# Performance work log

Hardware: AMD Instinct MI355X
Metric: run time of the kernel (lower is better)

## Reference

```python
import jax, jax.numpy as jnp
import numpy as np

N = 20000      # points
K = 16         # neighbor pairs per query per branch
M = N * K      # total pairs
C = 384        # embed_dim
H = 6          # num_heads
HD = C // H    # head_dim = 64
H1 = H // 2    # cartesian-branch heads
L = 24         # quant_grid_length (window 6.0 / quant 0.25)
Q = 0.25       # quant_size
LS = 24        # quant_grid_length_sphere (120 / 5)
QS = 5.0       # quant_size_sphere
A = 0.05 * 0.25  # exponential_split 'a'
SCALE = HD ** -0.5


def setup_inputs() -> dict:
    key = jax.random.key(0)
    ks = jax.random.split(key, 12)
    s = 0.02
    inp = {}
    inp["query_feats"] = jax.random.normal(ks[0], (N, C), jnp.float32)
    inp["xyz"] = jax.random.uniform(ks[1], (N, 3), jnp.float32, -3.0, 3.0)
    inp["index_0"] = jnp.repeat(jnp.arange(N, dtype=jnp.int32), K)
    inp["index_1"] = jax.random.randint(ks[2], (M,), 0, N, dtype=jnp.int32)
    inp["index_0_sphere"] = jnp.repeat(jnp.arange(N, dtype=jnp.int32), K)
    inp["index_1_sphere"] = jax.random.randint(ks[3], (M,), 0, N, dtype=jnp.int32)
    inp["W_qkv"] = jax.random.normal(ks[4], (C, 3 * C), jnp.float32) * s
    inp["b_qkv"] = jnp.zeros((3 * C,), jnp.float32)
    inp["W_proj"] = jax.random.normal(ks[5], (C, C), jnp.float32) * s
    inp["b_proj"] = jnp.zeros((C,), jnp.float32)
    inp["tq"] = jax.random.normal(ks[6], (2 * L - 1, 3, H1, HD), jnp.float32) * s
    inp["tk"] = jax.random.normal(ks[7], (2 * L - 1, 3, H1, HD), jnp.float32) * s
    inp["tv"] = jax.random.normal(ks[8], (2 * L - 1, 3, H1, HD), jnp.float32) * s
    inp["tq_s"] = jax.random.normal(ks[9], (2 * LS, 3, H - H1, HD), jnp.float32) * s
    inp["tk_s"] = jax.random.normal(ks[10], (2 * LS, 3, H - H1, HD), jnp.float32) * s
    inp["tv_s"] = jax.random.normal(ks[11], (2 * LS, 3, H - H1, HD), jnp.float32) * s
    return inp


def _cart2sphere(xyz):
    x, y, z = xyz[:, 0], xyz[:, 1], xyz[:, 2]
    theta = (jnp.arctan2(y, x) + np.pi) * (180.0 / np.pi)
    beta = jnp.arctan2(jnp.sqrt(x * x + y * y), z) * (180.0 / np.pi)
    r = jnp.sqrt(x * x + y * y + z * z)
    return jnp.stack([theta, beta, r], -1)


def _rel_idx_cart(xyz, i0, i1):
    rel = xyz[i0] - xyz[i1]  # [M,3]
    idx = jnp.floor(rel / Q).astype(jnp.int32) + (L - 1)
    return jnp.clip(idx, 0, 2 * L - 2)


def _rel_idx_sphere(sph, i0, i1):
    rel = sph[i0] - sph[i1]  # [M,3] (theta, beta, r)
    idx01 = jnp.clip(jnp.floor(rel[:, :2] / QS).astype(jnp.int32) + LS, 0, 2 * LS - 1)
    # exponential_split on radial dim
    r = rel[:, 2]
    ra = jnp.abs(r)
    flag = (r >= 0).astype(jnp.float32)
    idx = 2.0 * jnp.floor(jnp.log((ra + 2.0 * A) / A) / np.log(2.0)) - 2.0
    idx = idx + ((3.0 * jnp.exp2(jnp.floor(idx / 2.0)) - 2.0) * A <= ra).astype(jnp.float32)
    idx = idx * (2.0 * flag - 1.0) + (flag - 1.0)
    idx2 = jnp.clip(idx.astype(jnp.int32) + 24, 0, 2 * LS - 1)
    return jnp.concatenate([idx01, idx2[:, None]], 1)


def _branch(q, k, v, i0, i1, rel_idx, Tq, Tk, Tv):
    # q,k,v: [N,h,d]; i0/i1: [M]; rel_idx: [M,3]; tables: [R,3,h,d]
    qg = q[i0]  # [M,h,d]
    kg = k[i1]
    attn = jnp.einsum('mhd,mhd->mh', qg, kg)
    for dim in range(3):
        attn = attn + jnp.einsum('mhd,mhd->mh', qg, Tq[rel_idx[:, dim], dim])
        attn = attn + jnp.einsum('mhd,mhd->mh', kg, Tk[rel_idx[:, dim], dim])
    # segment softmax over queries (i0)
    seg_max = jax.ops.segment_max(attn, i0, num_segments=N)
    ex = jnp.exp(attn - seg_max[i0])
    p = ex / jax.ops.segment_sum(ex, i0, num_segments=N)[i0]  # [M,h]
    vg = v[i1] + Tv[rel_idx[:, 0], 0] + Tv[rel_idx[:, 1], 1] + Tv[rel_idx[:, 2], 2]
    return jax.ops.segment_sum(p[:, :, None] * vg, i0, num_segments=N)  # [N,h,d]


def reference(query_feats, xyz, index_0, index_1, index_0_sphere, index_1_sphere,
              W_qkv, b_qkv, W_proj, b_proj, tq, tk, tv, tq_s, tk_s, tv_s):
    i0 = index_0.astype(jnp.int32)
    i1 = index_1.astype(jnp.int32)
    i0s = index_0_sphere.astype(jnp.int32)
    i1s = index_1_sphere.astype(jnp.int32)
    qkv = (query_feats @ W_qkv + b_qkv).reshape(N, 3, H, HD)
    q = qkv[:, 0] * SCALE
    k = qkv[:, 1]
    v = qkv[:, 2]
    sph = _cart2sphere(xyz)
    ri = _rel_idx_cart(xyz, i0, i1)
    out1 = _branch(q[:, :H1], k[:, :H1], v[:, :H1], i0, i1, ri, tq, tk, tv)
    ri_s = _rel_idx_sphere(sph, i0s, i1s)
    out2 = _branch(q[:, H1:], k[:, H1:], v[:, H1:], i0s, i1s, ri_s, tq_s, tk_s, tv_s)
    x = jnp.concatenate([out1, out2], 1).reshape(N, C)
    return x @ W_proj + b_proj
```

## Files before the change

kernel.cpp:

```cpp
#include <hip/hip_runtime.h>
#include <hip/hip_bf16.h>

namespace {

constexpr int NP   = 20000;
constexpr int CD   = 384;
constexpr int QKVD = 1152;
constexpr int TC   = 47 * 3 * 3 * 64;
constexpr int TS   = 48 * 3 * 3 * 64;

constexpr int PB0 = NP * CD / 4 / 256;
constexpr int PB1 = PB0 + (QKVD / 32) * (CD / 32);
constexpr int PB2 = PB1 + (CD / 32) * (CD / 32);
constexpr int PB3 = PB2 + 27 * 7;

constexpr int ANB = 240;
constexpr int ANY = (NP + ANB - 1) / ANB;

typedef __attribute__((ext_vector_type(8))) short short8;
typedef __attribute__((ext_vector_type(4))) float f32x4;
typedef __attribute__((ext_vector_type(2))) float f32x2;

__device__ inline float f32_atan2(float y, float x) {
  return (float)atan2((double)y, (double)x);
}
__device__ inline float f32_log(float x) {
  return (float)log((double)x);
}

__device__ inline float bfl(unsigned u) {
  union { unsigned u; float f; } c; c.u = u << 16; return c.f;
}
__device__ inline float bfh(unsigned u) {
  union { unsigned u; float f; } c; c.u = u & 0xffff0000u; return c.f;
}
__device__ inline f32x2 up2(unsigned u) {
  f32x2 r;
  r.x = bfl(u);
  r.y = bfh(u);
  return r;
}
__device__ inline unsigned short f2bf(float x) {
  __hip_bfloat16 hb = __float2bfloat16(x);
  unsigned short u; __builtin_memcpy(&u, &hb, 2);
  return u;
}

#if __has_builtin(__builtin_amdgcn_fdot2_f32_bf16)
#define HAVE_BF16_DOT 1
typedef __attribute__((ext_vector_type(2))) __bf16 bf16x2_t;
__device__ inline float dot2bf(unsigned a, unsigned b, float c) {
  bf16x2_t av, bv;
  __builtin_memcpy(&av, &a, 4);
  __builtin_memcpy(&bv, &b, 4);
  return __builtin_amdgcn_fdot2_f32_bf16(av, bv, c, false);
}
#endif

__device__ inline void async16(const void* g, void* l) {
  __builtin_amdgcn_global_load_lds(
      (const __attribute__((address_space(1))) unsigned int*)g,
      (__attribute__((address_space(3))) unsigned int*)l,
      16, 0, 0);
}

__device__ inline uint4 tld(const char* t, int row, int bo) {
  return *(const uint4*)(t + row * 128 + (bo ^ ((row & 7) << 4)));
}
__device__ inline void tst(char* t, int row, int bo, uint4 v) {
  *(uint4*)(t + row * 128 + (bo ^ ((row & 7) << 4))) = v;
}

__global__ __launch_bounds__(256) void prep_all_k(const float* __restrict__ qf,
                                                  unsigned short* __restrict__ qf_b,
                                                  const float* __restrict__ Wqkv,
                                                  unsigned short* __restrict__ wqkvT,
                                                  const float* __restrict__ Wproj,
                                                  unsigned short* __restrict__ wprojT,
                                                  const float* __restrict__ tq,
                                                  const float* __restrict__ tk,
                                                  const float* __restrict__ tv,
                                                  const float* __restrict__ tqs,
                                                  const float* __restrict__ tks,
                                                  const float* __restrict__ tvs,
                                                  unsigned short* __restrict__ tq_b,
                                                  unsigned short* __restrict__ tk_b,
                                                  unsigned short* __restrict__ tv_b,
                                                  unsigned short* __restrict__ tqs_b,
                                                  unsigned short* __restrict__ tks_b,
                                                  unsigned short* __restrict__ tvs_b,
                                                  const float* __restrict__ xyz,
                                                  float* __restrict__ sph) {
  const int bid = blockIdx.x;
  const int tid = threadIdx.x;
  __shared__ float t[32][33];

  if (bid < PB0) {
    int i = (bid * 256 + tid) * 4;
    float4 v = *(const float4*)(qf + i);
    ushort4 o;
    o.x = f2bf(v.x); o.y = f2bf(v.y); o.z = f2bf(v.z); o.w = f2bf(v.w);
    *(ushort4*)(qf_b + i) = o;
  } else if (bid < PB2) {
    const float* in;
    unsigned short* out;
    int R, Cc, bx, by;
    if (bid < PB1) {
      in = Wqkv; out = wqkvT; R = CD; Cc = QKVD;
      int tt = bid - PB0; bx = tt % (QKVD / 32); by = tt / (QKVD / 32);
    } else {
      in = Wproj; out = wprojT; R = CD; Cc = CD;
      int tt = bid - PB1; bx = tt % (CD / 32); by = tt / (CD / 32);
    }
    const int c0 = bx * 32, r0 = by * 32;
    const int tx = tid & 31, ty = tid >> 5;
    #pragma unroll
    for (int i = 0; i < 32; i += 8)
      t[ty + i][tx] = in[(size_t)(r0 + ty + i) * Cc + (c0 + tx)];
    __syncthreads();
    #pragma unroll
    for (int i = 0; i < 32; i += 8)
      out[(size_t)(c0 + ty + i) * R + (r0 + tx)] = f2bf(t[tx][ty + i]);
  } else {
    const int tt = bid - PB2;
    const int bx = tt % 27, y = tt / 27;
    const int th = bx * 256 + tid;
    if (y < 6) {
      const float* in = (y == 0) ? tq : (y == 1) ? tk : (y == 2) ? tv
                      : (y == 3) ? tqs : (y == 4) ? tks : tvs;
      unsigned short* out = (y == 0) ? tq_b : (y == 1) ? tk_b : (y == 2) ? tv_b
                          : (y == 3) ? tqs_b : (y == 4) ? tks_b : tvs_b;
      const int n = (y < 3) ? TC : TS;
      int i = th * 4;
      if (i < n) {
        float4 v = *(const float4*)(in + i);
        ushort4 o;
        o.x = f2bf(v.x); o.y = f2bf(v.y); o.z = f2bf(v.z); o.w = f2bf(v.w);
        *(ushort4*)(out + i) = o;
      }
    } else {
#pragma clang fp contract(off)
      #pragma unroll
      for (int r = 0; r < 4; ++r) {
        int i = th * 4 + r;
        if (i < NP) {
          const float PIF = 3.14159265358979323846f;
          const float R2D = 57.29577951308232f;
          float x = xyz[i * 3 + 0], yy = xyz[i * 3 + 1], z = xyz[i * 3 + 2];
          float sxy = x * x + yy * yy;
          sph[i * 3 + 0] = (f32_atan2(yy, x) + PIF) * R2D;
          sph[i * 3 + 1] = f32_atan2(sqrtf(sxy), z) * R2D;
          sph[i * 3 + 2] = sqrtf(sxy + z * z);
        }
      }
    }
  }
}

__global__ __launch_bounds__(256) void bin_k(const float* __restrict__ xyz,
                                             const float* __restrict__ sph,
                                             const int* __restrict__ nb_c,
                                             const int* __restrict__ nb_s,
                                             int4* __restrict__ ebuf) {
#pragma clang fp contract(off)
  const int t = blockIdx.x * 256 + threadIdx.x;
  if (t >= 2 * NP * 16) return;
  const int b   = t / (NP * 16);
  const int rem = t - b * NP * 16;
  const int n   = rem >> 4;
  const int e   = rem & 15;
  int4 o;
  if (b == 0) {
    const int i1 = nb_c[n * 16 + e];
    const float rel[3] = {xyz[n * 3 + 0] - xyz[i1 * 3 + 0],
                          xyz[n * 3 + 1] - xyz[i1 * 3 + 1],
                          xyz[n * 3 + 2] - xyz[i1 * 3 + 2]};
    int r[3];
    #pragma unroll
    for (int dim = 0; dim < 3; ++dim) {
      int idx = (int)floorf(rel[dim] * 4.0f) + 23;
      idx = min(max(idx, 0), 46);
      r[dim] = idx * 3 + dim;
    }
    o.x = r[0]; o.y = r[1]; o.z = r[2]; o.w = i1;
  } else {
    const int i1 = nb_s[n * 16 + e];
    const float d0 = sph[n * 3 + 0] - sph[i1 * 3 + 0];
    const float d1 = sph[n * 3 + 1] - sph[i1 * 3 + 1];
    const float dr = sph[n * 3 + 2] - sph[i1 * 3 + 2];
    int i0a = (int)floorf(d0 / 5.0f) + 24;
    int i1a = (int)floorf(d1 / 5.0f) + 24;
    const float ra = fabsf(dr);
    const float flag = (dr >= 0.0f) ? 1.0f : 0.0f;
    const float tt = (ra + 0.025f) / 0.0125f;
    const float wv = f32_log(tt) / 0.69314718055994531f;
    float fidx = 2.0f * floorf(wv) - 2.0f;
    fidx += ((3.0f * exp2f(floorf(fidx * 0.5f)) - 2.0f) * 0.0125f <= ra) ? 1.0f : 0.0f;
    fidx = fidx * (2.0f * flag - 1.0f) + (flag - 1.0f);
    int i2a = (int)fidx + 24;
    o.x = min(max(i0a, 0), 47) * 3 + 0;
    o.y = min(max(i1a, 0), 47) * 3 + 1;
    o.z = min(max(i2a, 0), 47) * 3 + 2;
    o.w = i1;
  }
  ebuf[t] = o;
}

template <int MODE>
__global__ __launch_bounds__(256) void gemm_async_k(const short* __restrict__ A,
                                                    const short* __restrict__ BT,
                                                    const float* __restrict__ bias,
                                                    void* __restrict__ Cout,
                                                    int M, int Nn, int K) {
  __shared__ short As[3][128][32];
  __shared__ short Bs[3][128][32];
  const int tid  = threadIdx.x;

  const int NT  = Nn >> 7;
  const int nwg = gridDim.x;
  const int q = nwg >> 3, r = nwg & 7;
  const int xcd = blockIdx.x & 7, j = blockIdx.x >> 3;
  const int wg = (xcd < r ? xcd * (q + 1) : r * (q + 1) + (xcd - r) * q) + j;
  const int m0 = (wg / NT) * 128, n0 = (wg % NT) * 128;

  const int wave = tid >> 6, lane = tid & 63;
  const int wm   = (wave & 1) * 64, wn = (wave >> 1) * 64;
  const int quad = lane >> 4, l16 = lane & 15;
  const int srow = lane >> 2;
  const int scol = (lane & 3) * 8;

  f32x4 acc[4][4] = {};

  auto stage = [&](int buf, int k0) {
    #pragma unroll
    for (int c = 0; c < 2; ++c) {
      const int base = (wave + c * 4) * 16;
      async16(A + (size_t)(m0 + base + srow) * K + k0 + scol, &As[buf][base][0]);
      async16(BT + (size_t)(n0 + base + srow) * K + k0 + scol, &Bs[buf][base][0]);
    }
  };

  const int nt = K >> 5;
  stage(0, 0);
  stage(1, 32);
  for (int t = 0; t < nt; ++t) {
    const int cur = t % 3;
    if (t + 1 < nt) {
      asm volatile("s_waitcnt vmcnt(4)" ::: "memory");
    } else {
      asm volatile("s_waitcnt vmcnt(0)" ::: "memory");
    }
    __builtin_amdgcn_s_barrier();
    short8 af[4], bg[4];
    #pragma unroll
    for (int i = 0; i < 4; ++i) af[i] = *(const short8*)&As[cur][wm + i * 16 + l16][quad * 8];
    #pragma unroll
    for (int j2 = 0; j2 < 4; ++j2) bg[j2] = *(const short8*)&Bs[cur][wn + j2 * 16 + l16][quad * 8];
    #pragma unroll
    for (int i = 0; i < 4; ++i)
      #pragma unroll
      for (int j2 = 0; j2 < 4; ++j2)
        acc[i][j2] = __builtin_amdgcn_mfma_f32_16x16x32_bf16(af[i], bg[j2], acc[i][j2], 0, 0, 0);
    __builtin_amdgcn_s_barrier();
    if (t + 2 < nt) stage((t + 2) % 3, (t + 2) * 32);
  }

  #pragma unroll
  for (int i = 0; i < 4; ++i) {
    #pragma unroll
    for (int r2 = 0; r2 < 4; ++r2) {
      const int gm = m0 + wm + i * 16 + quad * 4 + r2;
      if (gm >= M) continue;
      #pragma unroll
      for (int j2 = 0; j2 < 4; ++j2) {
        const int gn = n0 + wn + j2 * 16 + l16;
        if (gn >= Nn) continue;
        float v = acc[i][j2][r2] + bias[gn];
        if (MODE == 0) {
          if (gn < 384) v *= 0.125f;
          ((unsigned short*)Cout)[(size_t)gm * Nn + gn] = f2bf(v);
        } else {
          ((float*)Cout)[(size_t)gm * Nn + gn] = v;
        }
      }
    }
  }
}

__device__ inline f32x2 dot8_pk(uint4 q, uint4 k, uint4 a0, uint4 a1, uint4 a2,
                                uint4 t0, uint4 t1, uint4 t2, f32x2 acc) {
  const unsigned* qp = &q.x;  const unsigned* kp = &k.x;
  const unsigned* a0p = &a0.x; const unsigned* a1p = &a1.x; const unsigned* a2p = &a2.x;
  const unsigned* t0p = &t0.x; const unsigned* t1p = &t1.x; const unsigned* t2p = &t2.x;
  #pragma unroll
  for (int w2 = 0; w2 < 4; ++w2) {
    f32x2 qf = up2(qp[w2]), kf = up2(kp[w2]);
    f32x2 tqs = up2(a0p[w2]) + up2(a1p[w2]) + up2(a2p[w2]);
    f32x2 tks = up2(t0p[w2]) + up2(t1p[w2]) + up2(t2p[w2]);
    acc += qf * (kf + tqs) + kf * tks;
  }
  return acc;
}

__device__ inline void acc4(f32x2* vc, uint4 vv, uint4 t0, uint4 t1, uint4 t2,
                            float pr) {
  f32x2 prv = {pr, pr};
  vc[0] += prv * (up2(vv.x) + up2(t0.x) + up2(t1.x) + up2(t2.x));
  vc[1] += prv * (up2(vv.y) + up2(t0.y) + up2(t1.y) + up2(t2.y));
  vc[2] += prv * (up2(vv.z) + up2(t0.z) + up2(t1.z) + up2(t2.z));
  vc[3] += prv * (up2(vv.w) + up2(t0.w) + up2(t1.w) + up2(t2.w));
}

__global__ __launch_bounds__(1024, 4) void attn_lds_k(const unsigned short* __restrict__ qkv,
                                                      const int4* __restrict__ ebuf,
                                                      const unsigned short* __restrict__ tq_c,
                                                      const unsigned short* __restrict__ tk_c,
                                                      const unsigned short* __restrict__ tv_c,
                                                      const unsigned short* __restrict__ tq_s,
                                                      const unsigned short* __restrict__ tk_s,
                                                      const unsigned short* __restrict__ tv_s,
                                                      unsigned short* __restrict__ xout) {
  __shared__ char s_tq[144 * 128];
  __shared__ char s_tk[144 * 128];
  __shared__ char s_tv[144 * 128];

  const int bh  = blockIdx.x;
  const int b   = bh / 3;
  const int hh  = bh % 3;
  const int wid = threadIdx.x >> 6, lane = threadIdx.x & 63;

  const unsigned short* gtq = b ? tq_s : tq_c;
  const unsigned short* gtk = b ? tk_s : tk_c;
  const unsigned short* gtv = b ? tv_s : tv_c;
  const int nrows = b ? 144 : 141;

  for (int i = threadIdx.x; i < nrows * 8; i += 1024) {
    const int row = i >> 3, c8 = i & 7;
    const int go = row * 192 + hh * 64 + c8 * 8;
    tst(s_tq, row, c8 * 16, *(const uint4*)(gtq + go));
    tst(s_tk, row, c8 * 16, *(const uint4*)(gtk + go));
    tst(s_tv, row, c8 * 16, *(const uint4*)(gtv + go));
  }
  __syncthreads();

  const int eg = lane >> 2, g = lane & 3;
  const int e8 = lane >> 3, c = lane & 7;
  const int node_end = min(blockIdx.y * ANB + ANB, NP);

  for (int node = blockIdx.y * ANB + wid; node < node_end; node += 16) {
    const int4* eb = ebuf + ((size_t)b * NP + node) * 16;

    const int4 E  = eb[eg];
    const int4 EA = eb[e8];
    const int4 EB = eb[e8 + 8];

    const unsigned short* qp = qkv + (size_t)node * QKVD + b * 192 + hh * 64 + g * 16;
    const uint4 qv0 = *(const uint4*)(qp);
    const uint4 qv1 = *(const uint4*)(qp + 8);
    const unsigned short* kp = qkv + (size_t)E.w * QKVD + 384 + b * 192 + hh * 64 + g * 16;
    const uint4 kv0 = *(const uint4*)(kp);
    const uint4 kv1 = *(const uint4*)(kp + 8);
    const int hc = hh * 64 + c * 8;
    const uint4 vA = *(const uint4*)(qkv + (size_t)EA.w * QKVD + 768 + b * 192 + hc);
    const uint4 vB = *(const uint4*)(qkv + (size_t)EB.w * QKVD + 768 + b * 192 + hc);

    const int bo = g * 32;
    const uint4 a00 = tld(s_tq, E.x, bo), a01 = tld(s_tq, E.x, bo + 16);
    const uint4 a10 = tld(s_tq, E.y, bo), a11 = tld(s_tq, E.y, bo + 16);
    const uint4 a20 = tld(s_tq, E.z, bo), a21 = tld(s_tq, E.z, bo + 16);
    const uint4 b00 = tld(s_tk, E.x, bo), b01 = tld(s_tk, E.x, bo + 16);
    const uint4 b10 = tld(s_tk, E.y, bo), b11 = tld(s_tk, E.y, bo + 16);
    const uint4 b20 = tld(s_tk, E.z, bo), b21 = tld(s_tk, E.z, bo + 16);

    float acc;
#ifdef HAVE_BF16_DOT
    float aqk = 0.0f, aq0 = 0.0f, aq1 = 0.0f, aq2 = 0.0f;
    float ak0 = 0.0f, ak1 = 0.0f, ak2 = 0.0f;
#define DOT7(qd, kd, a0d, a1d, a2d, b0d, b1d, b2d)                         \
    aqk = dot2bf(qd, kd, aqk);  aq0 = dot2bf(qd, a0d, aq0);                \
    aq1 = dot2bf(qd, a1d, aq1); aq2 = dot2bf(qd, a2d, aq2);                \
    ak0 = dot2bf(kd, b0d, ak0); ak1 = dot2bf(kd, b1d, ak1);                \
    ak2 = dot2bf(kd, b2d, ak2);
    DOT7(qv0.x, kv0.x, a00.x, a10.x, a20.x, b00.x, b10.x, b20.x)
    DOT7(qv0.y, kv0.y, a00.y, a10.y, a20.y, b00.y, b10.y, b20.y)
    DOT7(qv0.z, kv0.z, a00.z, a10.z, a20.z, b00.z, b10.z, b20.z)
    DOT7(qv0.w, kv0.w, a00.w, a10.w, a20.w, b00.w, b10.w, b20.w)
    DOT7(qv1.x, kv1.x, a01.x, a11.x, a21.x, b01.x, b11.x, b21.x)
    DOT7(qv1.y, kv1.y, a01.y, a11.y, a21.y, b01.y, b11.y, b21.y)
    DOT7(qv1.z, kv1.z, a01.z, a11.z, a21.z, b01.z, b11.z, b21.z)
    DOT7(qv1.w, kv1.w, a01.w, a11.w, a21.w, b01.w, b11.w, b21.w)
#undef DOT7
    acc = ((aqk + aq0) + (aq1 + aq2)) + ((ak0 + ak1) + ak2);
#else
    f32x2 acc2 = {0.0f, 0.0f};
    acc2 = dot8_pk(qv0, kv0, a00, a10, a20, b00, b10, b20, acc2);
    acc2 = dot8_pk(qv1, kv1, a01, a11, a21, b01, b11, b21, acc2);
    acc = acc2.x + acc2.y;
#endif
    acc += __shfl_xor(acc, 1);
    acc += __shfl_xor(acc, 2);

    float m = acc;
    #pragma unroll
    for (int off = 4; off <= 32; off <<= 1) m = fmaxf(m, __shfl_xor(m, off));
    float ex = __expf(acc - m);
    float s = ex;
    #pragma unroll
    for (int off = 4; off <= 32; off <<= 1) s += __shfl_xor(s, off);
    const float p = ex / s;

    const float pA = __shfl(p, e8 << 2);
    const float pB = __shfl(p, (e8 + 8) << 2);
    const int vbo = c * 16;
    const uint4 tA0 = tld(s_tv, EA.x, vbo);
    const uint4 tA1 = tld(s_tv, EA.y, vbo);
    const uint4 tA2 = tld(s_tv, EA.z, vbo);
    const uint4 tB0 = tld(s_tv, EB.x, vbo);
    const uint4 tB1 = tld(s_tv, EB.y, vbo);
    const uint4 tB2 = tld(s_tv, EB.z, vbo);

    f32x2 vc[4] = {{0.f, 0.f}, {0.f, 0.f}, {0.f, 0.f}, {0.f, 0.f}};
    acc4(vc, vA, tA0, tA1, tA2, pA);
    acc4(vc, vB, tB0, tB1, tB2, pB);

    #pragma unroll
    for (int q4 = 0; q4 < 4; ++q4) {
      #pragma unroll
      for (int off = 8; off <= 32; off <<= 1) {
        vc[q4].x += __shfl_xor(vc[q4].x, off);
        vc[q4].y += __shfl_xor(vc[q4].y, off);
      }
    }
    if (e8 == 0) {
      uint4 o;
      o.x = ((unsigned)f2bf(vc[0].y) << 16) | (unsigned)f2bf(vc[0].x);
      o.y = ((unsigned)f2bf(vc[1].y) << 16) | (unsigned)f2bf(vc[1].x);
      o.z = ((unsigned)f2bf(vc[2].y) << 16) | (unsigned)f2bf(vc[2].x);
      o.w = ((unsigned)f2bf(vc[3].y) << 16) | (unsigned)f2bf(vc[3].x);
      *(uint4*)(xout + (size_t)node * CD + (b * 3 + hh) * 64 + c * 8) = o;
    }
  }
}

}

extern "C" void kernel_launch(void* const* d_in, const int* in_sizes, int n_in,
                              void* d_out, int out_size, void* d_ws, size_t ws_size,
                              hipStream_t stream) {
  const float* qf    = (const float*)d_in[0];
  const float* xyz   = (const float*)d_in[1];
  const int*   i1c   = (const int*)d_in[3];
  const int*   i1s   = (const int*)d_in[5];
  const float* Wqkv  = (const float*)d_in[6];
  const float* bqkv  = (const float*)d_in[7];
  const float* Wproj = (const float*)d_in[8];
  const float* bproj = (const float*)d_in[9];
  const float* tq    = (const float*)d_in[10];
  const float* tk    = (const float*)d_in[11];
  const float* tv    = (const float*)d_in[12];
  const float* tqs   = (const float*)d_in[13];
  const float* tks   = (const float*)d_in[14];
  const float* tvs   = (const float*)d_in[15];

  char* w = (char*)d_ws;
  unsigned short* qf_b   = (unsigned short*)w; w += (size_t)NP * CD * 2;
  unsigned short* wqkvT  = (unsigned short*)w; w += (size_t)QKVD * CD * 2;
  unsigned short* wprojT = (unsigned short*)w; w += (size_t)CD * CD * 2;
  unsigned short* qkv_b  = (unsigned short*)w; w += (size_t)NP * QKVD * 2;
  unsigned short* x_b    = (unsigned short*)w; w += (size_t)NP * CD * 2;
  float*          sph    = (float*)w;          w += (size_t)NP * 3 * 4;
  unsigned short* tq_b   = (unsigned short*)w; w += (size_t)TC * 2;
  unsigned short* tk_b   = (unsigned short*)w; w += (size_t)TC * 2;
  unsigned short* tv_b   = (unsigned short*)w; w += (size_t)TC * 2;
  unsigned short* tqs_b  = (unsigned short*)w; w += (size_t)TS * 2;
  unsigned short* tks_b  = (unsigned short*)w; w += (size_t)TS * 2;
  unsigned short* tvs_b  = (unsigned short*)w; w += (size_t)TS * 2;
  int4*           ebuf   = (int4*)w;

  prep_all_k<<<PB3, 256, 0, stream>>>(qf, qf_b, Wqkv, wqkvT, Wproj, wprojT,
                                      tq, tk, tv, tqs, tks, tvs,
                                      tq_b, tk_b, tv_b, tqs_b, tks_b, tvs_b,
                                      xyz, sph);

  bin_k<<<(2 * NP * 16 + 255) / 256, 256, 0, stream>>>(xyz, sph, i1c, i1s, ebuf);

  gemm_async_k<0><<<((NP + 127) / 128) * (QKVD / 128), 256, 0, stream>>>(
      (const short*)qf_b, (const short*)wqkvT, bqkv, qkv_b, NP, QKVD, CD);

  attn_lds_k<<<dim3(6, ANY), 1024, 0, stream>>>(qkv_b, ebuf,
                                                tq_b, tk_b, tv_b,
                                                tqs_b, tks_b, tvs_b, x_b);

  gemm_async_k<1><<<((NP + 127) / 128) * (CD / 128), 256, 0, stream>>>(
      (const short*)x_b, (const short*)wprojT, bproj, d_out, NP, CD, CD);
}
```

Before: 281.9 us.

## Replace LDS-staged GEMM with direct global-to-register double-buffered fragment loads

The QKV and output-projection GEMMs no longer stage A/B tiles through LDS with async global-to-LDS copies and barriers. Each wave now loads its MFMA fragments straight from global memory into registers, double-buffered across K steps, with K fixed at 384 and the loop fully unrolled. This removes LDS traffic, barriers and waitcnt stalls. In exchange, waves sharing rows load them twice, and the per-lane 16-byte strided loads rely on L1/L2 caching.

```diff
diff --git a/kernel.cpp b/kernel.cpp
--- a/kernel.cpp
+++ b/kernel.cpp
@@ -56,13 +56,6 @@
   return __builtin_amdgcn_fdot2_f32_bf16(av, bv, c, false);
 }
 #endif
-
-__device__ inline void async16(const void* g, void* l) {
-  __builtin_amdgcn_global_load_lds(
-      (const __attribute__((address_space(1))) unsigned int*)g,
-      (__attribute__((address_space(3))) unsigned int*)l,
-      16, 0, 0);
-}
 
 __device__ inline uint4 tld(const char* t, int row, int bo) {
   return *(const uint4*)(t + row * 128 + (bo ^ ((row & 7) << 4)));
@@ -207,15 +200,13 @@
 }
 
 template <int MODE>
-__global__ __launch_bounds__(256) void gemm_async_k(const short* __restrict__ A,
-                                                    const short* __restrict__ BT,
-                                                    const float* __restrict__ bias,
-                                                    void* __restrict__ Cout,
-                                                    int M, int Nn, int K) {
-  __shared__ short As[3][128][32];
-  __shared__ short Bs[3][128][32];
-  const int tid  = threadIdx.x;
-
+__global__ __launch_bounds__(256) void gemm_direct_k(const short* __restrict__ A,
+                                                     const short* __restrict__ BT,
+                                                     const float* __restrict__ bias,
+                                                     void* __restrict__ Cout,
+                                                     int M, int Nn) {
+  constexpr int K = 384;
+  constexpr int NSTEP = K / 32;
   const int NT  = Nn >> 7;
   const int nwg = gridDim.x;
   const int q = nwg >> 3, r = nwg & 7;
@@ -223,47 +214,45 @@
   const int wg = (xcd < r ? xcd * (q + 1) : r * (q + 1) + (xcd - r) * q) + j;
   const int m0 = (wg / NT) * 128, n0 = (wg % NT) * 128;
 
+  const int tid  = threadIdx.x;
   const int wave = tid >> 6, lane = tid & 63;
   const int wm   = (wave & 1) * 64, wn = (wave >> 1) * 64;
   const int quad = lane >> 4, l16 = lane & 15;
-  const int srow = lane >> 2;
-  const int scol = (lane & 3) * 8;
+
+  const short* ap = A  + (size_t)(m0 + wm + l16) * K + quad * 8;
+  const short* bp = BT + (size_t)(n0 + wn + l16) * K + quad * 8;
 
   f32x4 acc[4][4] = {};
-
-  auto stage = [&](int buf, int k0) {
-    #pragma unroll
-    for (int c = 0; c < 2; ++c) {
-      const int base = (wave + c * 4) * 16;
-      async16(A + (size_t)(m0 + base + srow) * K + k0 + scol, &As[buf][base][0]);
-      async16(BT + (size_t)(n0 + base + srow) * K + k0 + scol, &Bs[buf][base][0]);
-    }
-  };
-
-  const int nt = K >> 5;
-  stage(0, 0);
-  stage(1, 32);
-  for (int t = 0; t < nt; ++t) {
-    const int cur = t % 3;
-    if (t + 1 < nt) {
-      asm volatile("s_waitcnt vmcnt(4)" ::: "memory");
-    } else {
-      asm volatile("s_waitcnt vmcnt(0)" ::: "memory");
-    }
-    __builtin_amdgcn_s_barrier();
-    short8 af[4], bg[4];
-    #pragma unroll
-    for (int i = 0; i < 4; ++i) af[i] = *(const short8*)&As[cur][wm + i * 16 + l16][quad * 8];
-    #pragma unroll
-    for (int j2 = 0; j2 < 4; ++j2) bg[j2] = *(const short8*)&Bs[cur][wn + j2 * 16 + l16][quad * 8];
-    #pragma unroll
-    for (int i = 0; i < 4; ++i)
-      #pragma unroll
-      for (int j2 = 0; j2 < 4; ++j2)
-        acc[i][j2] = __builtin_amdgcn_mfma_f32_16x16x32_bf16(af[i], bg[j2], acc[i][j2], 0, 0, 0);
-    __builtin_amdgcn_s_barrier();
-    if (t + 2 < nt) stage((t + 2) % 3, (t + 2) * 32);
-  }
+  short8 aA[4], bA[4], aB[4], bB[4];
+
+#define LDFR(as, bs, k0)                                                     \
+  do {                                                                       \
+    _Pragma("unroll")                                                        \
+    for (int i = 0; i < 4; ++i) {                                            \
+      as[i] = *(const short8*)(ap + (size_t)i * 16 * K + (k0));              \
+      bs[i] = *(const short8*)(bp + (size_t)i * 16 * K + (k0));              \
+    }                                                                        \
+  } while (0)
+#define MM16(as, bs)                                                         \
+  do {                                                                       \
+    _Pragma("unroll")                                                        \
+    for (int i = 0; i < 4; ++i)                                              \
+      _Pragma("unroll")                                                      \
+      for (int j2 = 0; j2 < 4; ++j2)                                         \
+        acc[i][j2] = __builtin_amdgcn_mfma_f32_16x16x32_bf16(                \
+            as[i], bs[j2], acc[i][j2], 0, 0, 0);                             \
+  } while (0)
+
+  LDFR(aA, bA, 0);
+  #pragma unroll
+  for (int t = 0; t < NSTEP; t += 2) {
+    if (t + 1 < NSTEP) LDFR(aB, bB, (t + 1) * 32);
+    MM16(aA, bA);
+    if (t + 2 < NSTEP) LDFR(aA, bA, (t + 2) * 32);
+    MM16(aB, bB);
+  }
+#undef LDFR
+#undef MM16
 
   #pragma unroll
   for (int i = 0; i < 4; ++i) {
@@ -484,13 +473,13 @@
 
   bin_k<<<(2 * NP * 16 + 255) / 256, 256, 0, stream>>>(xyz, sph, i1c, i1s, ebuf);
 
-  gemm_async_k<0><<<((NP + 127) / 128) * (QKVD / 128), 256, 0, stream>>>(
-      (const short*)qf_b, (const short*)wqkvT, bqkv, qkv_b, NP, QKVD, CD);
+  gemm_direct_k<0><<<((NP + 127) / 128) * (QKVD / 128), 256, 0, stream>>>(
+      (const short*)qf_b, (const short*)wqkvT, bqkv, qkv_b, NP, QKVD);
 
   attn_lds_k<<<dim3(6, ANY), 1024, 0, stream>>>(qkv_b, ebuf,
                                                 tq_b, tk_b, tv_b,
                                                 tqs_b, tks_b, tvs_b, x_b);
 
-  gemm_async_k<1><<<((NP + 127) / 128) * (CD / 128), 256, 0, stream>>>(
-      (const short*)x_b, (const short*)wprojT, bproj, d_out, NP, CD, CD);
-}
+  gemm_direct_k<1><<<((NP + 127) / 128) * (CD / 128), 256, 0, stream>>>(
+      (const short*)x_b, (const short*)wprojT, bproj, d_out, NP, CD);
+}
```

Result: slower. 337.6 us (+19.8%).
